# Performance work log

Hardware: AMD Instinct MI355X
Metric: run time of the kernel (lower is better)

## Reference

```python
import jax, jax.numpy as jnp
import numpy as np

D_K = 128
D_V = 128
SEQ_LEN = 2048


def setup_inputs() -> dict:
    key = jax.random.key(0)
    kq, kk, kv = jax.random.split(key, 3)
    q = jax.random.normal(kq, (SEQ_LEN, D_K), dtype=jnp.float32)
    k = jax.random.normal(kk, (SEQ_LEN, D_K), dtype=jnp.float32)
    v = jax.random.normal(kv, (SEQ_LEN, D_V), dtype=jnp.float32)
    return {"q": q, "k": k, "v": v}


def _step(carry, qkv):
    J, Svv, Sqv, Sqq, l = carry
    q, k, v = qkv
    l = l + 1
    fl = l.astype(J.dtype)
    # update_correlations: running means of outer products
    Svv = (fl - 1.0) / fl * Svv + jnp.outer(v, v) / fl
    Sqv = (fl - 1.0) / fl * Sqv + jnp.outer(q, v) / fl
    Sqq = (fl - 1.0) / fl * Sqq + jnp.outer(q, q) / fl

    first = l == 1

    # ecological params (J: [d_v, d_k], Sqv: [d_k, d_v], Sqq: [d_k, d_k])
    s_J = jnp.einsum('vk,kv->', J, Sqv)            # trace(J @ Sigma_qv)
    s_l = k @ Sqv @ v
    A_JJ = jnp.einsum('vk,kj,vj->', J, Sqq, J)     # trace(J Sqq J^T)
    A_ll = (v @ v) * (k @ Sqq @ k)
    A_Jl = v @ J @ Sqq @ k

    # safe denominators (unused branches must not produce NaN under where)
    A_JJ_s = jnp.where(first | (A_JJ == 0), 1.0, A_JJ)
    A_ll_s = jnp.where(first | (A_ll == 0), 1.0, A_ll)
    denom = A_JJ * A_ll - A_Jl ** 2
    denom_s = jnp.where(first | (denom == 0), 1.0, denom)

    margin = s_l - A_Jl * (s_J / A_JJ_s)

    wf = (A_ll * s_J - A_Jl * s_l) / denom_s
    wi = (A_JJ * s_l - A_Jl * s_J) / denom_s
    # nonnegativity constraints (check omega_i first, as in the source)
    wf_c = jnp.where(wi <= 0, s_J / A_JJ_s, jnp.where(wf <= 0, 0.0, wf))
    wi_c = jnp.where(wi <= 0, 0.0, jnp.where(wf <= 0, s_l / A_ll_s, wi))

    do_update = margin > 0
    vk = jnp.outer(v, k)
    J_upd = jnp.where(do_update, wf_c * J + wi_c * vk, J)
    J_new = jnp.where(first, vk, J_upd)
    updated = first | do_update

    # compute_cost with updated J and correlations
    cost = (0.5 * jnp.trace(Svv)
            - jnp.einsum('vk,kv->', J_new, Sqv)
            + 0.5 * jnp.einsum('vk,kj,vj->', J_new, Sqq, J_new))

    return (J_new, Svv, Sqv, Sqq, l), (cost, updated)


def _run(q, k, v):
    d_k, d_v = q.shape[-1], v.shape[-1]
    init = (jnp.zeros((d_v, d_k), q.dtype),
            jnp.zeros((d_v, d_v), q.dtype),
            jnp.zeros((d_k, d_v), q.dtype),
            jnp.zeros((d_k, d_k), q.dtype),
            jnp.int32(0))
    (J, _, _, _, _), (costs, updated) = jax.lax.scan(_step, init, (q, k, v))
    return costs, updated, J


def reference(q, k, v):
    return _run(q, k, v)
```

## Files before the change

kernel.cpp:

```cpp
#include <hip/hip_runtime.h>

#define SEQ 2048
#define D 128

typedef float v2f __attribute__((ext_vector_type(2)));
typedef float v4f __attribute__((ext_vector_type(4)));
#define LO2(v) __builtin_shufflevector(v, v, 0, 1)
#define HI2(v) __builtin_shufflevector(v, v, 2, 3)

__global__ __launch_bounds__(256) void precompute_kernel(
    const float* __restrict__ q, const float* __restrict__ k, const float* __restrict__ v,
    float* __restrict__ U, float* __restrict__ sl, float* __restrict__ kqq,
    float* __restrict__ vv, float* __restrict__ kq_adj, float* __restrict__ vv_adj,
    float* __restrict__ kU_adj, double* __restrict__ invl)
{
    const int s = blockIdx.x;
    const int tid = threadIdx.x;

    __shared__ float ks[D];
    __shared__ float vs[D];
    __shared__ float alpha[SEQ];
    __shared__ float red[8];
    __shared__ float upart[256];

    if (tid < D) ks[tid] = k[s * D + tid];
    else if (tid < 2 * D) vs[tid - D] = v[s * D + (tid - D)];
    __syncthreads();

    float p_a2 = 0.f, p_ab = 0.f;
    for (int i = tid; i <= s; i += 256) {
        const float4* qr = (const float4*)(q + (size_t)i * D);
        const float4* vr = (const float4*)(v + (size_t)i * D);
        float a = 0.f, b = 0.f;
#pragma unroll
        for (int j = 0; j < D / 4; ++j) {
            float4 q4 = qr[j];
            float4 v4 = vr[j];
            a += q4.x * ks[4 * j + 0] + q4.y * ks[4 * j + 1] + q4.z * ks[4 * j + 2] + q4.w * ks[4 * j + 3];
            b += v4.x * vs[4 * j + 0] + v4.y * vs[4 * j + 1] + v4.z * vs[4 * j + 2] + v4.w * vs[4 * j + 3];
        }
        alpha[i] = a;
        p_a2 += a * a;
        p_ab += a * b;
        if (i == s) vv[s] = b;
    }
#pragma unroll
    for (int off = 1; off < 64; off <<= 1) {
        p_a2 += __shfl_xor(p_a2, off);
        p_ab += __shfl_xor(p_ab, off);
    }
    const int wid = tid >> 6;
    if ((tid & 63) == 0) { red[wid] = p_a2; red[4 + wid] = p_ab; }
    __syncthreads();
    if (tid == 0) {
        kqq[s] = red[0] + red[1] + red[2] + red[3];
        sl[s]  = red[4] + red[5] + red[6] + red[7];
        invl[s] = 1.0 / (double)(s + 1);
    }

    if (tid < 64) {
        if (s + 1 < SEQ) {
            float p2 = ks[tid] * q[(size_t)(s + 1) * D + tid]
                     + ks[tid + 64] * q[(size_t)(s + 1) * D + 64 + tid];
#pragma unroll
            for (int off = 1; off < 64; off <<= 1) p2 += __shfl_xor(p2, off);
            if (tid == 0) kq_adj[s + 1] = p2;
        }
        if (s == 0 && tid == 0) { kq_adj[0] = 0.f; kU_adj[0] = 0.f; vv_adj[0] = 0.f; }
    } else if (tid < 128 && s > 0) {
        const int t2 = tid - 64;
        float p2 = vs[t2] * v[(size_t)(s - 1) * D + t2]
                 + vs[t2 + 64] * v[(size_t)(s - 1) * D + 64 + t2];
#pragma unroll
        for (int off = 1; off < 64; off <<= 1) p2 += __shfl_xor(p2, off);
        if (t2 == 0) vv_adj[s] = p2;
    }

    const int c = tid & (D - 1);
    const int h = tid >> 7;
    float a0 = 0.f, a1 = 0.f, a2 = 0.f, a3 = 0.f;
    int i = h;
    for (; i + 6 <= s; i += 8) {
        a0 = fmaf(q[(size_t)(i    ) * D + c], alpha[i    ], a0);
        a1 = fmaf(q[(size_t)(i + 2) * D + c], alpha[i + 2], a1);
        a2 = fmaf(q[(size_t)(i + 4) * D + c], alpha[i + 4], a2);
        a3 = fmaf(q[(size_t)(i + 6) * D + c], alpha[i + 6], a3);
    }
    for (; i <= s; i += 2) a0 = fmaf(q[(size_t)i * D + c], alpha[i], a0);
    upart[tid] = (a0 + a1) + (a2 + a3);
    __syncthreads();

    float kup = 0.f;
    if (tid < D) {
        const float uv = upart[tid] + upart[tid + D];
        U[(size_t)s * D + tid] = uv;
        if (s > 0) kup = uv * k[(size_t)(s - 1) * D + tid];
    }
#pragma unroll
    for (int off = 1; off < 64; off <<= 1) kup += __shfl_xor(kup, off);
    if (tid == 0)  red[0] = kup;
    if (tid == 64) red[1] = kup;
    __syncthreads();
    if (s > 0 && tid == 0) kU_adj[s] = red[0] + red[1];
}

#define DPP_ADD(x, ctrl) \
    ((x) + __int_as_float(__builtin_amdgcn_update_dpp(0, __float_as_int(x), (ctrl), 0xf, 0xf, true)))
#define REDUCE16(x) do { x = DPP_ADD(x, 0xB1); x = DPP_ADD(x, 0x4E); \
                         x = DPP_ADD(x, 0x141); x = DPP_ADD(x, 0x140); } while (0)

#define BARRIER() do { asm volatile("s_waitcnt lgkmcnt(0)" ::: "memory"); \
                       __builtin_amdgcn_s_barrier(); \
                       __builtin_amdgcn_sched_barrier(0); } while (0)

__global__ __launch_bounds__(1024, 4) void scan_kernel(
    const float* __restrict__ q, const float* __restrict__ k, const float* __restrict__ v,
    const float* __restrict__ U, const float* __restrict__ sl_arr,
    const float* __restrict__ kqq_arr, const float* __restrict__ vv_arr,
    const float* __restrict__ kq_adj, const float* __restrict__ vv_adj,
    const float* __restrict__ kU_adj, const double* __restrict__ invl_arr,
    float* __restrict__ out)
{
    const int tid  = threadIdx.x;
    const int lane = tid & 63;
    const int w    = __builtin_amdgcn_readfirstlane(tid >> 6);
    (void)kq_adj; (void)vv_adj; (void)kU_adj;

    __shared__ float ring[3][4][160];
    __shared__ __align__(16) float wred[3][32][4];
    __shared__ __align__(16) float fsl[SEQ];
    __shared__ __align__(16) float fkq[SEQ];
    __shared__ __align__(16) float fvv[SEQ];
    __shared__ __align__(16) double finv[SEQ];

    const bool isj     = (tid >= 512);
    const int  jw      = w - 8;
    const int  i16     = lane & 15;
    const int  r4      = lane >> 4;
    const int  o       = 20 * (i16 >> 1) + 8 * (i16 & 1);
    const int  rb      = (jw << 4) + (r4 << 2);
    const int  vo      = 20 * jw + (r4 << 2);

    const bool stager  = (tid >= 128) && (tid < 512);
    const int  which   = (tid >> 7) - 1;
    const int  sidx    = tid & 127;
    const int  widx    = ((sidx >> 4) * 20) + (sidx & 15);

    const bool vstager = (tid >= 64) && (tid < 128);
    const int  s2      = tid & 63;
    const int  vc0     = 2 * s2;
    const int  vwidx   = 20 * (vc0 >> 4) + (vc0 & 15);

    v2f jA0 = {0.f, 0.f}, jA1 = jA0, jA2 = jA0, jA3 = jA0;
    v2f jB0 = jA0, jB1 = jA0, jB2 = jA0, jB3 = jA0;
    v2f jC0 = jA0, jC1 = jA0, jC2 = jA0, jC3 = jA0;
    v2f jD0 = jA0, jD1 = jA0, jD2 = jA0, jD3 = jA0;

    float gs[3] = {0.f, 0.f, 0.f};
    v2f   gv[3] = {{0.f,0.f},{0.f,0.f},{0.f,0.f}};

    if (tid < 512) {
        ((float4*)fsl)[tid] = ((const float4*)sl_arr)[tid];
        ((float4*)fvv)[tid] = ((const float4*)vv_arr)[tid];
    } else {
        ((float4*)fkq)[tid - 512] = ((const float4*)kqq_arr)[tid - 512];
    }
    ((double2*)finv)[tid] = ((const double2*)invl_arr)[tid];

    if (stager) {
        if (which == 0) {
            ring[0][0][widx] = q[(size_t)1 * D + sidx];
            ring[1][0][widx] = q[(size_t)2 * D + sidx];
            gs[2] = q[(size_t)3 * D + sidx];
            gs[0] = q[(size_t)4 * D + sidx];
            gs[1] = q[(size_t)5 * D + sidx];
        } else if (which == 1) {
            ring[0][1][widx] = U[(size_t)1 * D + sidx];
            ring[1][1][widx] = U[(size_t)2 * D + sidx];
            gs[2] = U[(size_t)3 * D + sidx];
            gs[0] = U[(size_t)4 * D + sidx];
            gs[1] = U[(size_t)5 * D + sidx];
        } else {
            ring[0][2][widx] = k[(size_t)1 * D + sidx];
            ring[1][2][widx] = k[(size_t)2 * D + sidx];
            gs[2] = k[(size_t)3 * D + sidx];
            gs[0] = k[(size_t)4 * D + sidx];
            gs[1] = k[(size_t)5 * D + sidx];
        }
    } else if (vstager) {
        *(v2f*)&ring[0][3][vwidx] = *(const v2f*)&v[(size_t)1 * D + vc0];
        *(v2f*)&ring[1][3][vwidx] = *(const v2f*)&v[(size_t)2 * D + vc0];
        gv[2] = *(const v2f*)&v[(size_t)3 * D + vc0];
        gv[0] = *(const v2f*)&v[(size_t)4 * D + vc0];
        gv[1] = *(const v2f*)&v[(size_t)5 * D + vc0];
    }

    double SJ = 0.0, AJJ = 0.0, trSvv = 0.0;
    if (isj) {
        const v4f v0  = *(const v4f*)&v[rb];
        const v4f Ka0 = *(const v4f*)&k[8 * i16];
        const v4f Kb0 = *(const v4f*)&k[8 * i16 + 4];
        const v2f k0_ = LO2(Ka0), k1_ = HI2(Ka0), k2_ = LO2(Kb0), k3_ = HI2(Kb0);
        const v2f wA = {v0.x, v0.x}, wB = {v0.y, v0.y};
        const v2f wC = {v0.z, v0.z}, wD = {v0.w, v0.w};
        jA0 = wA * k0_; jA1 = wA * k1_; jA2 = wA * k2_; jA3 = wA * k3_;
        jB0 = wB * k0_; jB1 = wB * k1_; jB2 = wB * k2_; jB3 = wB * k3_;
        jC0 = wC * k0_; jC1 = wC * k1_; jC2 = wC * k2_; jC3 = wC * k3_;
        jD0 = wD * k0_; jD1 = wD * k1_; jD2 = wD * k2_; jD3 = wD * k3_;
        const double vv0 = (double)vv_arr[0];
        SJ    = (double)sl_arr[0];
        AJJ   = vv0 * (double)kqq_arr[0];
        trSvv = vv0;
    }
    if (tid == 0) {
        const double sl0 = (double)sl_arr[0];
        const double kq0 = (double)kqq_arr[0];
        const double vv0 = (double)vv_arr[0];
        out[0] = (float)((0.5 * vv0 - sl0 + 0.5 * vv0 * kq0) * invl_arr[0]);
        out[SEQ] = 1.f;
    }
    __syncthreads();

#define STEP_BODY(I, P, PN, PW)                                               \
{                                                                             \
    float c_sl = 0.f, c_kq = 0.f, c_vv = 0.f;                                 \
    double c_inv = 0.0;                                                       \
    v2f k0_ = {0.f, 0.f}, k1_ = k0_, k2_ = k0_, k3_ = k0_;                    \
    v4f vn4 = {0.f, 0.f, 0.f, 0.f};                                           \
    if (isj) {                                                                \
        c_sl = fsl[(I) + 1]; c_kq = fkq[(I) + 1]; c_vv = fvv[(I) + 1];        \
        c_inv = finv[(I) + 1];                                                \
        const v4f Qa = ((const v4f*)&ring[P][0][o])[0];                       \
        const v4f Qb = ((const v4f*)&ring[P][0][o])[1];                       \
        const v4f Ua = ((const v4f*)&ring[P][1][o])[0];                       \
        const v4f Ub = ((const v4f*)&ring[P][1][o])[1];                       \
        const v4f Ka = ((const v4f*)&ring[P][2][o])[0];                       \
        const v4f Kb = ((const v4f*)&ring[P][2][o])[1];                       \
        vn4 = *((const v4f*)&ring[P][3][vo]);                                 \
        k0_ = LO2(Ka); k1_ = HI2(Ka); k2_ = LO2(Kb); k3_ = HI2(Kb);           \
        const v2f q0 = LO2(Qa), q1 = HI2(Qa), q2 = LO2(Qb), q3 = HI2(Qb);     \
        v2f aA = jA0 * q0, aB = jB0 * q0, aC = jC0 * q0, aD = jD0 * q0;       \
        aA = __builtin_elementwise_fma(jA1, q1, aA);                          \
        aB = __builtin_elementwise_fma(jB1, q1, aB);                          \
        aC = __builtin_elementwise_fma(jC1, q1, aC);                          \
        aD = __builtin_elementwise_fma(jD1, q1, aD);                          \
        aA = __builtin_elementwise_fma(jA2, q2, aA);                          \
        aB = __builtin_elementwise_fma(jB2, q2, aB);                          \
        aC = __builtin_elementwise_fma(jC2, q2, aC);                          \
        aD = __builtin_elementwise_fma(jD2, q2, aD);                          \
        aA = __builtin_elementwise_fma(jA3, q3, aA);                          \
        aB = __builtin_elementwise_fma(jB3, q3, aB);                          \
        aC = __builtin_elementwise_fma(jC3, q3, aC);                          \
        aD = __builtin_elementwise_fma(jD3, q3, aD);                          \
        float YqA = aA.x + aA.y, YqB = aB.x + aB.y;                           \
        float YqC = aC.x + aC.y, YqD = aD.x + aD.y;                           \
        const v2f u0 = LO2(Ua), u1 = HI2(Ua), u2 = LO2(Ub), u3 = HI2(Ub);     \
        v2f bA = jA0 * u0, bB = jB0 * u0, bC = jC0 * u0, bD = jD0 * u0;       \
        bA = __builtin_elementwise_fma(jA1, u1, bA);                          \
        bB = __builtin_elementwise_fma(jB1, u1, bB);                          \
        bC = __builtin_elementwise_fma(jC1, u1, bC);                          \
        bD = __builtin_elementwise_fma(jD1, u1, bD);                          \
        bA = __builtin_elementwise_fma(jA2, u2, bA);                          \
        bB = __builtin_elementwise_fma(jB2, u2, bB);                          \
        bC = __builtin_elementwise_fma(jC2, u2, bC);                          \
        bD = __builtin_elementwise_fma(jD2, u2, bD);                          \
        bA = __builtin_elementwise_fma(jA3, u3, bA);                          \
        bB = __builtin_elementwise_fma(jB3, u3, bB);                          \
        bC = __builtin_elementwise_fma(jC3, u3, bC);                          \
        bD = __builtin_elementwise_fma(jD3, u3, bD);                          \
        float YwA = bA.x + bA.y, YwB = bB.x + bB.y;                           \
        float YwC = bC.x + bC.y, YwD = bD.x + bD.y;                           \
        REDUCE16(YqA); REDUCE16(YqB); REDUCE16(YqC); REDUCE16(YqD);           \
        REDUCE16(YwA); REDUCE16(YwB); REDUCE16(YwC); REDUCE16(YwD);           \
        const float z1 = (vn4.x * YqA + vn4.y * YqB) + (vn4.z * YqC + vn4.w * YqD); \
        const float z2 = (YqA * YqA + YqB * YqB) + (YqC * YqC + YqD * YqD);   \
        const float z4 = (vn4.x * YwA + vn4.y * YwB) + (vn4.z * YwC + vn4.w * YwD); \
        if ((lane & 15) == 15)                                                \
            *(float4*)&wred[P][(jw << 2) | r4][0] = make_float4(z1, z2, z4, 0.f); \
    }                                                                         \
    BARRIER();                                                                \
    if (stager) {                                                             \
        ring[PW][which][widx] = gs[PW];                                       \
        const int t6 = ((I) + 6 < SEQ) ? (I) + 6 : SEQ - 1;                   \
        gs[PW] = (which == 0) ? q[(size_t)t6 * D + sidx]                      \
               : (which == 1) ? U[(size_t)t6 * D + sidx]                      \
                              : k[(size_t)t6 * D + sidx];                     \
    } else if (vstager) {                                                     \
        *(v2f*)&ring[PW][3][vwidx] = gv[PW];                                  \
        const int t6 = ((I) + 6 < SEQ) ? (I) + 6 : SEQ - 1;                   \
        gv[PW] = *(const v2f*)&v[(size_t)t6 * D + vc0];                       \
    } else if (isj) {                                                         \
        const float4 wa = *(const float4*)&wred[P][lane & 15][0];             \
        const float4 wb = *(const float4*)&wred[P][16 + (lane & 15)][0];      \
        float wx = wa.x + wb.x, wy = wa.y + wb.y, wz = wa.z + wb.z;           \
        REDUCE16(wx);                                                         \
        REDUCE16(wy);                                                         \
        REDUCE16(wz);                                                         \
        trSvv += (double)c_vv;                                                \
        SJ    += (double)wx;                                                  \
        AJJ   += (double)wy;                                                  \
        const double AJl_ = (double)wz;                                       \
        const double s_l  = (double)c_sl;                                     \
        const double A_ll = (double)c_vv * (double)c_kq;                      \
        const double AJJ_s  = (AJJ == 0.0)  ? 1.0 : AJJ;                      \
        const double A_ll_s = (A_ll == 0.0) ? 1.0 : A_ll;                     \
        const double denom   = AJJ * A_ll - AJl_ * AJl_;                      \
        const double denom_s = (denom == 0.0) ? 1.0 : denom;                  \
        const double rden = 1.0 / denom_s;                                    \
        const double wf = (A_ll * SJ - AJl_ * s_l) * rden;                    \
        const double wi = (AJJ * s_l - AJl_ * SJ) * rden;                     \
        double wf_c, wi_c;                                                    \
        if (wi <= 0.0)      { wf_c = SJ / AJJ_s;  wi_c = 0.0; }               \
        else if (wf <= 0.0) { wf_c = 0.0;         wi_c = s_l / A_ll_s; }      \
        else                { wf_c = wf;          wi_c = wi; }                \
        const bool do_update = (s_l * AJJ_s - AJl_ * SJ) > 0.0;               \
        int mode = 0;                                                         \
        if (do_update) {                                                      \
            mode = 1;                                                         \
            const double nSJ = wf_c * SJ + wi_c * s_l;                        \
            AJJ = wf_c * wf_c * AJJ + 2.0 * wf_c * wi_c * AJl_                \
                + wi_c * wi_c * A_ll;                                         \
            SJ = nSJ;                                                         \
            const float uwf = (float)wf_c;                                    \
            const float uwi = (float)wi_c;                                    \
            const v2f wf2 = {uwf, uwf};                                       \
            const float sA = uwi * vn4.x, sB = uwi * vn4.y;                   \
            const float sC = uwi * vn4.z, sD = uwi * vn4.w;                   \
            const v2f wA = {sA, sA}, wB = {sB, sB};                           \
            const v2f wC = {sC, sC}, wD = {sD, sD};                           \
            jA0 = __builtin_elementwise_fma(jA0, wf2, wA * k0_);              \
            jA1 = __builtin_elementwise_fma(jA1, wf2, wA * k1_);              \
            jA2 = __builtin_elementwise_fma(jA2, wf2, wA * k2_);              \
            jA3 = __builtin_elementwise_fma(jA3, wf2, wA * k3_);              \
            jB0 = __builtin_elementwise_fma(jB0, wf2, wB * k0_);              \
            jB1 = __builtin_elementwise_fma(jB1, wf2, wB * k1_);              \
            jB2 = __builtin_elementwise_fma(jB2, wf2, wB * k2_);              \
            jB3 = __builtin_elementwise_fma(jB3, wf2, wB * k3_);              \
            jC0 = __builtin_elementwise_fma(jC0, wf2, wC * k0_);              \
            jC1 = __builtin_elementwise_fma(jC1, wf2, wC * k1_);              \
            jC2 = __builtin_elementwise_fma(jC2, wf2, wC * k2_);              \
            jC3 = __builtin_elementwise_fma(jC3, wf2, wC * k3_);              \
            jD0 = __builtin_elementwise_fma(jD0, wf2, wD * k0_);              \
            jD1 = __builtin_elementwise_fma(jD1, wf2, wD * k1_);              \
            jD2 = __builtin_elementwise_fma(jD2, wf2, wD * k2_);              \
            jD3 = __builtin_elementwise_fma(jD3, wf2, wD * k3_);              \
        }                                                                     \
        if (w == 8) {                                                         \
            const float cost = (float)((0.5 * trSvv - SJ + 0.5 * AJJ) * c_inv); \
            if (lane == 0) {                                                  \
                out[(I) + 1] = cost;                                          \
                out[SEQ + (I) + 1] = mode ? 1.f : 0.f;                        \
            }                                                                 \
        }                                                                     \
    }                                                                         \
}

    for (int i = 0; i + 2 < SEQ - 1; i += 3) {
        STEP_BODY(i,     0, 1, 2)
        STEP_BODY(i + 1, 1, 2, 0)
        STEP_BODY(i + 2, 2, 0, 1)
    }
    STEP_BODY(SEQ - 2, 0, 1, 2)
#undef STEP_BODY

    if (isj) {
        float* jb = out + 2 * SEQ + (size_t)rb * D + 8 * i16;
        *(v4f*)(jb + 0)         = __builtin_shufflevector(jA0, jA1, 0, 1, 2, 3);
        *(v4f*)(jb + 4)         = __builtin_shufflevector(jA2, jA3, 0, 1, 2, 3);
        *(v4f*)(jb + D + 0)     = __builtin_shufflevector(jB0, jB1, 0, 1, 2, 3);
        *(v4f*)(jb + D + 4)     = __builtin_shufflevector(jB2, jB3, 0, 1, 2, 3);
        *(v4f*)(jb + 2 * D + 0) = __builtin_shufflevector(jC0, jC1, 0, 1, 2, 3);
        *(v4f*)(jb + 2 * D + 4) = __builtin_shufflevector(jC2, jC3, 0, 1, 2, 3);
        *(v4f*)(jb + 3 * D + 0) = __builtin_shufflevector(jD0, jD1, 0, 1, 2, 3);
        *(v4f*)(jb + 3 * D + 4) = __builtin_shufflevector(jD2, jD3, 0, 1, 2, 3);
    }
}

extern "C" void kernel_launch(void* const* d_in, const int* in_sizes, int n_in,
                              void* d_out, int out_size, void* d_ws, size_t ws_size,
                              hipStream_t stream) {
    (void)in_sizes; (void)n_in; (void)out_size; (void)ws_size;
    const float* q = (const float*)d_in[0];
    const float* k = (const float*)d_in[1];
    const float* v = (const float*)d_in[2];
    float* out = (float*)d_out;

    float* U      = (float*)d_ws;
    float* sl     = U + (size_t)SEQ * D;
    float* kqq    = sl + SEQ;
    float* vv     = kqq + SEQ;
    float* kq_adj = vv + SEQ;
    float* vv_adj = kq_adj + SEQ;
    float* kU_adj = vv_adj + SEQ;
    double* invl  = (double*)(kU_adj + SEQ);

    precompute_kernel<<<SEQ, 256, 0, stream>>>(q, k, v, U, sl, kqq, vv,
                                               kq_adj, vv_adj, kU_adj, invl);
    scan_kernel<<<1, 1024, 0, stream>>>(q, k, v, U, sl, kqq, vv,
                                        kq_adj, vv_adj, kU_adj, invl, out);
}
```

Baseline: 2.606 ms.

## Process two scan steps per barrier round with deferred rank-2 J updates

Restructures the sequential scan so each round handles two timesteps. The precompute kernel now emits cross-step dot products (k·q, v·v, k·U at lags 1–3), which lets both steps' scalar decisions be derived from one batch of mat-vec reductions. The J update is deferred and applied as a fused rank-2 update. A Newton-refined hardware double reciprocal replaces the division. This halves the number of serial barrier rounds, at the cost of more LDS, more registers, extra precompute work and more complex algebra that could diverge numerically.

```diff
diff --git a/kernel.cpp b/kernel.cpp
--- a/kernel.cpp
+++ b/kernel.cpp
@@ -12,7 +12,8 @@
     const float* __restrict__ q, const float* __restrict__ k, const float* __restrict__ v,
     float* __restrict__ U, float* __restrict__ sl, float* __restrict__ kqq,
     float* __restrict__ vv, float* __restrict__ kq_adj, float* __restrict__ vv_adj,
-    float* __restrict__ kU_adj, double* __restrict__ invl)
+    float* __restrict__ kU_adj, double* __restrict__ invl,
+    float* __restrict__ kq_d, float* __restrict__ vv_d, float* __restrict__ kU_d)
 {
     const int s = blockIdx.x;
     const int tid = threadIdx.x;
@@ -59,21 +60,27 @@
     }
 
     if (tid < 64) {
-        if (s + 1 < SEQ) {
-            float p2 = ks[tid] * q[(size_t)(s + 1) * D + tid]
-                     + ks[tid + 64] * q[(size_t)(s + 1) * D + 64 + tid];
+        for (int d = 1; d <= 3; ++d) {
+            if (s + d < SEQ) {
+                float p2 = ks[tid] * q[(size_t)(s + d) * D + tid]
+                         + ks[tid + 64] * q[(size_t)(s + d) * D + 64 + tid];
 #pragma unroll
-            for (int off = 1; off < 64; off <<= 1) p2 += __shfl_xor(p2, off);
-            if (tid == 0) kq_adj[s + 1] = p2;
+                for (int off = 1; off < 64; off <<= 1) p2 += __shfl_xor(p2, off);
+                if (tid == 0) kq_d[(size_t)(s + d) * 3 + (d - 1)] = p2;
+            }
         }
         if (s == 0 && tid == 0) { kq_adj[0] = 0.f; kU_adj[0] = 0.f; vv_adj[0] = 0.f; }
-    } else if (tid < 128 && s > 0) {
+    } else if (tid < 128) {
         const int t2 = tid - 64;
-        float p2 = vs[t2] * v[(size_t)(s - 1) * D + t2]
-                 + vs[t2 + 64] * v[(size_t)(s - 1) * D + 64 + t2];
+        for (int d = 1; d <= 3; ++d) {
+            if (s - d >= 0) {
+                float p2 = vs[t2] * v[(size_t)(s - d) * D + t2]
+                         + vs[t2 + 64] * v[(size_t)(s - d) * D + 64 + t2];
 #pragma unroll
-        for (int off = 1; off < 64; off <<= 1) p2 += __shfl_xor(p2, off);
-        if (t2 == 0) vv_adj[s] = p2;
+                for (int off = 1; off < 64; off <<= 1) p2 += __shfl_xor(p2, off);
+                if (t2 == 0) vv_d[(size_t)s * 3 + (d - 1)] = p2;
+            }
+        }
     }
 
     const int c = tid & (D - 1);
@@ -90,18 +97,33 @@
     upart[tid] = (a0 + a1) + (a2 + a3);
     __syncthreads();
 
+    float uvv = 0.f;
     float kup = 0.f;
     if (tid < D) {
-        const float uv = upart[tid] + upart[tid + D];
-        U[(size_t)s * D + tid] = uv;
-        if (s > 0) kup = uv * k[(size_t)(s - 1) * D + tid];
+        uvv = upart[tid] + upart[tid + D];
+        U[(size_t)s * D + tid] = uvv;
+        if (s > 0) kup = uvv * k[(size_t)(s - 1) * D + tid];
     }
 #pragma unroll
     for (int off = 1; off < 64; off <<= 1) kup += __shfl_xor(kup, off);
     if (tid == 0)  red[0] = kup;
     if (tid == 64) red[1] = kup;
     __syncthreads();
-    if (s > 0 && tid == 0) kU_adj[s] = red[0] + red[1];
+    if (s > 0 && tid == 0) {
+        kU_adj[s] = red[0] + red[1];
+        kU_d[(size_t)s * 3 + 0] = red[0] + red[1];
+    }
+    for (int d = 2; d <= 3; ++d) {
+        float kd_ = 0.f;
+        if (tid < D && s - d >= 0) kd_ = uvv * k[(size_t)(s - d) * D + tid];
+#pragma unroll
+        for (int off = 1; off < 64; off <<= 1) kd_ += __shfl_xor(kd_, off);
+        __syncthreads();
+        if (tid == 0)  red[0] = kd_;
+        if (tid == 64) red[1] = kd_;
+        __syncthreads();
+        if (s - d >= 0 && tid == 0) kU_d[(size_t)s * 3 + (d - 1)] = red[0] + red[1];
+    }
 }
 
 #define DPP_ADD(x, ctrl) \
@@ -113,257 +135,364 @@
                        __builtin_amdgcn_s_barrier(); \
                        __builtin_amdgcn_sched_barrier(0); } while (0)
 
+static __device__ inline double fast_rcp(double d) {
+    double r;
+    asm("v_rcp_f64 %0, %1" : "=v"(r) : "v"(d));
+    double e = __builtin_fma(-d, r, 1.0); r = __builtin_fma(r, e, r);
+    e = __builtin_fma(-d, r, 1.0); r = __builtin_fma(r, e, r);
+    return r;
+}
+
 __global__ __launch_bounds__(1024, 4) void scan_kernel(
     const float* __restrict__ q, const float* __restrict__ k, const float* __restrict__ v,
     const float* __restrict__ U, const float* __restrict__ sl_arr,
     const float* __restrict__ kqq_arr, const float* __restrict__ vv_arr,
-    const float* __restrict__ kq_adj, const float* __restrict__ vv_adj,
-    const float* __restrict__ kU_adj, const double* __restrict__ invl_arr,
+    const float* __restrict__ qd_arr, const float* __restrict__ vvd_arr,
+    const float* __restrict__ kud_arr, const double* __restrict__ invl_arr,
     float* __restrict__ out)
 {
     const int tid  = threadIdx.x;
     const int lane = tid & 63;
     const int w    = __builtin_amdgcn_readfirstlane(tid >> 6);
-    (void)kq_adj; (void)vv_adj; (void)kU_adj;
-
-    __shared__ float ring[3][4][160];
-    __shared__ __align__(16) float wred[3][32][4];
-    __shared__ __align__(16) float fsl[SEQ];
-    __shared__ __align__(16) float fkq[SEQ];
-    __shared__ __align__(16) float fvv[SEQ];
+
+    __shared__ float ring[3][8][160];
+    __shared__ __align__(16) float wred[3][32][12];
+    __shared__ __align__(16) float decLDS[3][4];
+    __shared__ float fsl[SEQ];
+    __shared__ float fkq[SEQ];
+    __shared__ float fvv[SEQ];
+    __shared__ float fqd[SEQ * 3];
+    __shared__ float fvd[SEQ * 3];
+    __shared__ float fkd[SEQ * 3];
     __shared__ __align__(16) double finv[SEQ];
 
-    const bool isj     = (tid >= 512);
-    const int  jw      = w - 8;
-    const int  i16     = lane & 15;
-    const int  r4      = lane >> 4;
-    const int  o       = 20 * (i16 >> 1) + 8 * (i16 & 1);
-    const int  rb      = (jw << 4) + (r4 << 2);
-    const int  vo      = 20 * jw + (r4 << 2);
-
-    const bool stager  = (tid >= 128) && (tid < 512);
-    const int  which   = (tid >> 7) - 1;
-    const int  sidx    = tid & 127;
-    const int  widx    = ((sidx >> 4) * 20) + (sidx & 15);
-
-    const bool vstager = (tid >= 64) && (tid < 128);
-    const int  s2      = tid & 63;
-    const int  vc0     = 2 * s2;
-    const int  vwidx   = 20 * (vc0 >> 4) + (vc0 & 15);
+    const bool isj = (tid >= 512);
+    const int  jw  = w - 8;
+    const int  i16 = lane & 15;
+    const int  r4  = lane >> 4;
+    const int  o   = 20 * (i16 >> 1) + 8 * (i16 & 1);
+    const int  rb  = (jw << 4) + (r4 << 2);
+    const int  vo  = 20 * jw + (r4 << 2);
+
+    const bool stager = (tid >= 64 && tid < 256) || (tid >= 320 && tid < 512);
+    const int  st     = (tid < 256) ? tid - 64 : tid - 128;
+
+    if (tid < 512) {
+        ((float4*)fsl)[tid] = ((const float4*)sl_arr)[tid];
+        ((float4*)fkq)[tid] = ((const float4*)kqq_arr)[tid];
+        ((float4*)fvv)[tid] = ((const float4*)vv_arr)[tid];
+    }
+    ((double2*)finv)[tid] = ((const double2*)invl_arr)[tid];
+    for (int i = tid; i < SEQ * 3 / 4; i += 1024) {
+        ((float4*)fqd)[i] = ((const float4*)qd_arr)[i];
+        ((float4*)fvd)[i] = ((const float4*)vvd_arr)[i];
+        ((float4*)fkd)[i] = ((const float4*)kud_arr)[i];
+    }
 
     v2f jA0 = {0.f, 0.f}, jA1 = jA0, jA2 = jA0, jA3 = jA0;
     v2f jB0 = jA0, jB1 = jA0, jB2 = jA0, jB3 = jA0;
     v2f jC0 = jA0, jC1 = jA0, jC2 = jA0, jC3 = jA0;
     v2f jD0 = jA0, jD1 = jA0, jD2 = jA0, jD3 = jA0;
-
-    float gs[3] = {0.f, 0.f, 0.f};
-    v2f   gv[3] = {{0.f,0.f},{0.f,0.f},{0.f,0.f}};
-
-    if (tid < 512) {
-        ((float4*)fsl)[tid] = ((const float4*)sl_arr)[tid];
-        ((float4*)fvv)[tid] = ((const float4*)vv_arr)[tid];
-    } else {
-        ((float4*)fkq)[tid - 512] = ((const float4*)kqq_arr)[tid - 512];
-    }
-    ((double2*)finv)[tid] = ((const double2*)invl_arr)[tid];
+    v4f Q1a = {0,0,0,0}, Q1b = Q1a, Q2a = Q1a, Q2b = Q1a;
+    v4f U1a = Q1a, U1b = Q1a, U2a = Q1a, U2b = Q1a;
+    v4f kA1a = Q1a, kA1b = Q1a, kA2a = Q1a, kA2b = Q1a;
+    v4f kB1a = Q1a, kB1b = Q1a, kB2a = Q1a, kB2b = Q1a;
+    v4f vA1 = Q1a, vA2 = Q1a, vB1 = Q1a, vB2 = Q1a;
+
+    float g0[3] = {0, 0, 0}, g1[3] = {0, 0, 0}, g2[3] = {0, 0, 0};
+
+    double SJ = 0.0, AJJ = 0.0, trSvv = 0.0;
+    double fa = 1.0, ga = 0.0, fb = 1.0, gb = 0.0;
+
+#define MATVEC(Xa, Xb, RA, RB, RC, RD)                                        \
+    {                                                                         \
+        const v2f x0 = LO2(Xa), x1 = HI2(Xa), x2 = LO2(Xb), x3 = HI2(Xb);     \
+        v2f tA = jA0 * x0, tB = jB0 * x0, tC = jC0 * x0, tD = jD0 * x0;       \
+        tA = __builtin_elementwise_fma(jA1, x1, tA);                          \
+        tB = __builtin_elementwise_fma(jB1, x1, tB);                          \
+        tC = __builtin_elementwise_fma(jC1, x1, tC);                          \
+        tD = __builtin_elementwise_fma(jD1, x1, tD);                          \
+        tA = __builtin_elementwise_fma(jA2, x2, tA);                          \
+        tB = __builtin_elementwise_fma(jB2, x2, tB);                          \
+        tC = __builtin_elementwise_fma(jC2, x2, tC);                          \
+        tD = __builtin_elementwise_fma(jD2, x2, tD);                          \
+        tA = __builtin_elementwise_fma(jA3, x3, tA);                          \
+        tB = __builtin_elementwise_fma(jB3, x3, tB);                          \
+        tC = __builtin_elementwise_fma(jC3, x3, tC);                          \
+        tD = __builtin_elementwise_fma(jD3, x3, tD);                          \
+        RA = tA.x + tA.y; RB = tB.x + tB.y; RC = tC.x + tC.y; RD = tD.x + tD.y; \
+    }
+
+#define DOTPHASE(P_)                                                          \
+    {                                                                         \
+        float Yq1A, Yq1B, Yq1C, Yq1D, Yq2A, Yq2B, Yq2C, Yq2D;                 \
+        float W1A, W1B, W1C, W1D, W2A, W2B, W2C, W2D;                         \
+        MATVEC(Q1a, Q1b, Yq1A, Yq1B, Yq1C, Yq1D)                              \
+        MATVEC(Q2a, Q2b, Yq2A, Yq2B, Yq2C, Yq2D)                              \
+        MATVEC(U1a, U1b, W1A, W1B, W1C, W1D)                                  \
+        MATVEC(U2a, U2b, W2A, W2B, W2C, W2D)                                  \
+        REDUCE16(Yq1A); REDUCE16(Yq1B); REDUCE16(Yq1C); REDUCE16(Yq1D);       \
+        REDUCE16(Yq2A); REDUCE16(Yq2B); REDUCE16(Yq2C); REDUCE16(Yq2D);       \
+        float pb11 = vB1.x * Yq1A + vB1.y * Yq1B + vB1.z * Yq1C + vB1.w * Yq1D; \
+        float pb21 = Yq1A * Yq1A + Yq1B * Yq1B + Yq1C * Yq1C + Yq1D * Yq1D;   \
+        float pb41 = vB1.x * W1A + vB1.y * W1B + vB1.z * W1C + vB1.w * W1D;   \
+        REDUCE16(pb41);                                                       \
+        float pg11 = vA1.x * Yq1A + vA1.y * Yq1B + vA1.z * Yq1C + vA1.w * Yq1D; \
+        float pg21 = vA2.x * Yq1A + vA2.y * Yq1B + vA2.z * Yq1C + vA2.w * Yq1D; \
+        float pb12 = vB2.x * Yq2A + vB2.y * Yq2B + vB2.z * Yq2C + vB2.w * Yq2D; \
+        float pb22 = Yq2A * Yq2A + Yq2B * Yq2B + Yq2C * Yq2C + Yq2D * Yq2D;   \
+        float pb42 = vB2.x * W2A + vB2.y * W2B + vB2.z * W2C + vB2.w * W2D;   \
+        REDUCE16(pb42);                                                       \
+        float pg12 = vA1.x * Yq2A + vA1.y * Yq2B + vA1.z * Yq2C + vA1.w * Yq2D; \
+        float pg22 = vA2.x * Yq2A + vA2.y * Yq2B + vA2.z * Yq2C + vA2.w * Yq2D; \
+        float pg3  = vB1.x * Yq2A + vB1.y * Yq2B + vB1.z * Yq2C + vB1.w * Yq2D; \
+        if ((lane & 15) == 15) {                                              \
+            const int e_ = (jw << 2) | r4;                                    \
+            *(float4*)&wred[P_][e_][0] = make_float4(pb11, pb21, pb41, pg11); \
+            *(float4*)&wred[P_][e_][4] = make_float4(pg21, pb12, pb22, pb42); \
+            *(float4*)&wred[P_][e_][8] = make_float4(pg12, pg22, pg3, 0.f);   \
+        }                                                                     \
+    }
+
+#define J_UPDATE(PW_)                                                         \
+    {                                                                         \
+        const float4 df_ = *(const float4*)&decLDS[PW_][0];                   \
+        const float F_ = df_.x, Ga_ = df_.y, Gb_ = df_.z;                     \
+        if (!(F_ == 1.f && Ga_ == 0.f && Gb_ == 0.f)) {                       \
+            const v2f F2_ = {F_, F_};                                         \
+            const v2f k10 = LO2(kA1a), k11 = HI2(kA1a), k12 = LO2(kA1b), k13 = HI2(kA1b); \
+            const v2f k20 = LO2(kA2a), k21 = HI2(kA2a), k22 = LO2(kA2b), k23 = HI2(kA2b); \
+            { const float w1 = Ga_ * vA1.x, w2 = Gb_ * vA2.x;                 \
+              const v2f w1_ = {w1, w1}, w2_ = {w2, w2};                       \
+              jA0 = __builtin_elementwise_fma(jA0, F2_, __builtin_elementwise_fma(w1_, k10, w2_ * k20)); \
+              jA1 = __builtin_elementwise_fma(jA1, F2_, __builtin_elementwise_fma(w1_, k11, w2_ * k21)); \
+              jA2 = __builtin_elementwise_fma(jA2, F2_, __builtin_elementwise_fma(w1_, k12, w2_ * k22)); \
+              jA3 = __builtin_elementwise_fma(jA3, F2_, __builtin_elementwise_fma(w1_, k13, w2_ * k23)); } \
+            { const float w1 = Ga_ * vA1.y, w2 = Gb_ * vA2.y;                 \
+              const v2f w1_ = {w1, w1}, w2_ = {w2, w2};                       \
+              jB0 = __builtin_elementwise_fma(jB0, F2_, __builtin_elementwise_fma(w1_, k10, w2_ * k20)); \
+              jB1 = __builtin_elementwise_fma(jB1, F2_, __builtin_elementwise_fma(w1_, k11, w2_ * k21)); \
+              jB2 = __builtin_elementwise_fma(jB2, F2_, __builtin_elementwise_fma(w1_, k12, w2_ * k22)); \
+              jB3 = __builtin_elementwise_fma(jB3, F2_, __builtin_elementwise_fma(w1_, k13, w2_ * k23)); } \
+            { const float w1 = Ga_ * vA1.z, w2 = Gb_ * vA2.z;                 \
+              const v2f w1_ = {w1, w1}, w2_ = {w2, w2};                       \
+              jC0 = __builtin_elementwise_fma(jC0, F2_, __builtin_elementwise_fma(w1_, k10, w2_ * k20)); \
+              jC1 = __builtin_elementwise_fma(jC1, F2_, __builtin_elementwise_fma(w1_, k11, w2_ * k21)); \
+              jC2 = __builtin_elementwise_fma(jC2, F2_, __builtin_elementwise_fma(w1_, k12, w2_ * k22)); \
+              jC3 = __builtin_elementwise_fma(jC3, F2_, __builtin_elementwise_fma(w1_, k13, w2_ * k23)); } \
+            { const float w1 = Ga_ * vA1.w, w2 = Gb_ * vA2.w;                 \
+              const v2f w1_ = {w1, w1}, w2_ = {w2, w2};                       \
+              jD0 = __builtin_elementwise_fma(jD0, F2_, __builtin_elementwise_fma(w1_, k10, w2_ * k20)); \
+              jD1 = __builtin_elementwise_fma(jD1, F2_, __builtin_elementwise_fma(w1_, k11, w2_ * k21)); \
+              jD2 = __builtin_elementwise_fma(jD2, F2_, __builtin_elementwise_fma(w1_, k12, w2_ * k22)); \
+              jD3 = __builtin_elementwise_fma(jD3, F2_, __builtin_elementwise_fma(w1_, k13, w2_ * k23)); } \
+        }                                                                     \
+    }
+
+#define DECIDE(S_L, A_LL, AJL, FO, GO, MO)                                    \
+    {                                                                         \
+        const double s_l_ = (S_L), A_ll_ = (A_LL), AJl_ = (AJL);              \
+        const double AJJ_s_ = (AJJ == 0.0) ? 1.0 : AJJ;                       \
+        const double A_ll_s_ = (A_ll_ == 0.0) ? 1.0 : A_ll_;                  \
+        const double denom_ = AJJ * A_ll_ - AJl_ * AJl_;                      \
+        const double denom_s_ = (denom_ == 0.0) ? 1.0 : denom_;               \
+        const double rden_ = fast_rcp(denom_s_);                              \
+        const double wf_ = (A_ll_ * SJ - AJl_ * s_l_) * rden_;                \
+        const double wi_ = (AJJ * s_l_ - AJl_ * SJ) * rden_;                  \
+        double wfc_, wic_;                                                    \
+        if (wi_ <= 0.0)      { wfc_ = SJ / AJJ_s_;  wic_ = 0.0; }             \
+        else if (wf_ <= 0.0) { wfc_ = 0.0;          wic_ = s_l_ / A_ll_s_; }  \
+        else                 { wfc_ = wf_;          wic_ = wi_; }             \
+        if ((s_l_ * AJJ_s_ - AJl_ * SJ) > 0.0) {                              \
+            MO = 1;                                                           \
+            const double nSJ_ = wfc_ * SJ + wic_ * s_l_;                      \
+            AJJ = wfc_ * wfc_ * AJJ + 2.0 * wfc_ * wic_ * AJl_                \
+                + wic_ * wic_ * A_ll_;                                        \
+            SJ = nSJ_; FO = wfc_; GO = wic_;                                  \
+        } else { MO = 0; FO = 1.0; GO = 0.0; }                                \
+    }
+
+#define DECIDER(R, P_, PW_, LAST)                                             \
+    {                                                                         \
+        const int s1 = 2 * (R) + 1;                                           \
+        const int s2c = ((LAST)) ? SEQ - 1 : 2 * (R) + 2;                     \
+        const int la = lane & 15;                                             \
+        const float4 e0 = *(const float4*)&wred[PW_][la][0];                  \
+        const float4 e1 = *(const float4*)&wred[PW_][la][4];                  \
+        const float4 e2 = *(const float4*)&wred[PW_][la][8];                  \
+        const float4 h0 = *(const float4*)&wred[PW_][16 + la][0];             \
+        const float4 h1 = *(const float4*)&wred[PW_][16 + la][4];             \
+        const float4 h2 = *(const float4*)&wred[PW_][16 + la][8];             \
+        float B1_1 = e0.x + h0.x, B2_1 = e0.y + h0.y, B4_1 = e0.z + h0.z;     \
+        float G1_1 = e0.w + h0.w, G2_1 = e1.x + h1.x, B1_2 = e1.y + h1.y;     \
+        float B2_2 = e1.z + h1.z, B4_2 = e1.w + h1.w, G1_2 = e2.x + h2.x;     \
+        float G2_2 = e2.y + h2.y, G3f = e2.z + h2.z;                          \
+        REDUCE16(B1_1); REDUCE16(B2_1); REDUCE16(B4_1); REDUCE16(G1_1);       \
+        REDUCE16(G2_1); REDUCE16(B1_2); REDUCE16(B2_2); REDUCE16(B4_2);       \
+        REDUCE16(G1_2); REDUCE16(G2_2); REDUCE16(G3f);                        \
+        const int ia = (s1 >= 2) ? s1 - 2 : 0;                                \
+        const double vva = (double)fvv[ia];                                   \
+        const double vvb = (double)fvv[s1 - 1];                               \
+        const double vab = (double)fvd[(s1 - 1) * 3 + 0];                     \
+        const double qd1_1 = (double)fqd[s1 * 3 + 0], qd1_2 = (double)fqd[s1 * 3 + 1]; \
+        const double vd1_1 = (double)fvd[s1 * 3 + 0], vd1_2 = (double)fvd[s1 * 3 + 1]; \
+        const double kd1_1 = (double)fkd[s1 * 3 + 0], kd1_2 = (double)fkd[s1 * 3 + 1]; \
+        const double sl1 = (double)fsl[s1], kq1 = (double)fkq[s1], vv1 = (double)fvv[s1]; \
+        const double qd2_1 = (double)fqd[s2c * 3 + 0], qd2_2 = (double)fqd[s2c * 3 + 1], qd2_3 = (double)fqd[s2c * 3 + 2]; \
+        const double vd2_1 = (double)fvd[s2c * 3 + 0], vd2_2 = (double)fvd[s2c * 3 + 1], vd2_3 = (double)fvd[s2c * 3 + 2]; \
+        const double kd2_1 = (double)fkd[s2c * 3 + 0], kd2_2 = (double)fkd[s2c * 3 + 1], kd2_3 = (double)fkd[s2c * 3 + 2]; \
+        const double sl2 = (double)fsl[s2c], kq2 = (double)fkq[s2c], vv2 = (double)fvv[s2c]; \
+        const double inv1 = finv[s1], inv2 = finv[s2c];                       \
+        const double A = fa * fb, Ca = fb * ga, Cb = gb;                      \
+        const double z1 = A * (double)B1_1 + Ca * (vd1_2 * qd1_2)             \
+                        + Cb * (vd1_1 * qd1_1);                               \
+        const double z2 = A * A * (double)B2_1                                \
+                        + Ca * Ca * qd1_2 * qd1_2 * vva                       \
+                        + Cb * Cb * qd1_1 * qd1_1 * vvb                       \
+                        + 2.0 * A * (Ca * qd1_2 * (double)G1_1                \
+                                     + Cb * qd1_1 * (double)G2_1)             \
+                        + 2.0 * Ca * Cb * qd1_2 * qd1_1 * vab;                \
+        const double z4 = A * (double)B4_1 + Ca * vd1_2 * kd1_2               \
+                        + Cb * vd1_1 * kd1_1;                                 \
+        SJ += z1; AJJ += z2; trSvv += vv1;                                    \
+        double f1, g1; int mode1;                                             \
+        DECIDE(sl1, vv1 * kq1, z4, f1, g1, mode1)                             \
+        const double cost1 = (0.5 * trSvv - SJ + 0.5 * AJJ) * inv1;           \
+        const double A2 = f1 * A, Ca2 = f1 * Ca, Cb2 = f1 * Cb, Cc2 = g1;     \
+        double f2 = 1.0, g2 = 0.0; int mode2 = 0; double cost2 = 0.0;         \
+        if (!(LAST)) {                                                        \
+            const double y1 = A2 * (double)B1_2 + Ca2 * vd2_3 * qd2_3         \
+                            + Cb2 * vd2_2 * qd2_2 + Cc2 * vd2_1 * qd2_1;      \
+            const double y2 = A2 * A2 * (double)B2_2                          \
+                            + Ca2 * Ca2 * qd2_3 * qd2_3 * vva                 \
+                            + Cb2 * Cb2 * qd2_2 * qd2_2 * vvb                 \
+                            + Cc2 * Cc2 * qd2_1 * qd2_1 * vv1                 \
+                            + 2.0 * A2 * (Ca2 * qd2_3 * (double)G1_2          \
+                                          + Cb2 * qd2_2 * (double)G2_2        \
+                                          + Cc2 * qd2_1 * (double)G3f)        \
+                            + 2.0 * (Ca2 * Cb2 * qd2_3 * qd2_2 * vab          \
+                                     + Ca2 * Cc2 * qd2_3 * qd2_1 * vd1_2      \
+                                     + Cb2 * Cc2 * qd2_2 * qd2_1 * vd1_1);    \
+            const double y4 = A2 * (double)B4_2 + Ca2 * vd2_3 * kd2_3         \
+                            + Cb2 * vd2_2 * kd2_2 + Cc2 * vd2_1 * kd2_1;      \
+            SJ += y1; AJJ += y2; trSvv += vv2;                                \
+            DECIDE(sl2, vv2 * kq2, y4, f2, g2, mode2)                         \
+            cost2 = (0.5 * trSvv - SJ + 0.5 * AJJ) * inv2;                    \
+        }                                                                     \
+        fa = f1; ga = g1; fb = f2; gb = g2;                                   \
+        if (lane == 0) {                                                      \
+            out[s1] = (float)cost1; out[SEQ + s1] = mode1 ? 1.f : 0.f;        \
+            if (!(LAST)) {                                                    \
+                out[s2c] = (float)cost2; out[SEQ + s2c] = mode2 ? 1.f : 0.f;  \
+            }                                                                 \
+            *(float4*)&decLDS[P_][0] = make_float4(                           \
+                (float)(f1 * f2), (float)(g1 * f2), (float)g2, 0.f);          \
+        }                                                                     \
+    }
+
+#define ST_ONE(SLOT, GARR, R, PW_)                                            \
+    { const int s_ = (SLOT); const int a_ = s_ >> 7, c_ = s_ & 127;           \
+      const int wix = (c_ >> 4) * 20 + (c_ & 15);                             \
+      ring[PW_][a_][wix] = GARR[PW_];                                         \
+      const float* b_ = (a_ < 2) ? q : (a_ < 4) ? U : (a_ < 6) ? k : v;       \
+      int stp = 2 * ((R) + 6) + 1 + (a_ & 1);                                 \
+      if (stp > SEQ - 1) stp = SEQ - 1;                                       \
+      GARR[PW_] = b_[(size_t)stp * D + c_]; }
+
+#define STAGE(R, PW_)                                                         \
+    {                                                                         \
+        ST_ONE(st, g0, R, PW_)                                                \
+        ST_ONE(st + 384, g1, R, PW_)                                          \
+        if (st < 256) ST_ONE(st + 768, g2, R, PW_)                            \
+    }
+
+#define ROUND(R, P_, PN_, PW_, LAST)                                          \
+    {                                                                         \
+        if (isj) {                                                            \
+            J_UPDATE(PW_)                                                     \
+            vA1 = vB1; vA2 = vB2;                                             \
+            kA1a = kB1a; kA1b = kB1b; kA2a = kB2a; kA2b = kB2b;               \
+            Q1a = ((const v4f*)&ring[P_][0][o])[0];                           \
+            Q1b = ((const v4f*)&ring[P_][0][o])[1];                           \
+            Q2a = ((const v4f*)&ring[P_][1][o])[0];                           \
+            Q2b = ((const v4f*)&ring[P_][1][o])[1];                           \
+            U1a = ((const v4f*)&ring[P_][2][o])[0];                           \
+            U1b = ((const v4f*)&ring[P_][2][o])[1];                           \
+            U2a = ((const v4f*)&ring[P_][3][o])[0];                           \
+            U2b = ((const v4f*)&ring[P_][3][o])[1];                           \
+            kB1a = ((const v4f*)&ring[P_][4][o])[0];                          \
+            kB1b = ((const v4f*)&ring[P_][4][o])[1];                          \
+            kB2a = ((const v4f*)&ring[P_][5][o])[0];                          \
+            kB2b = ((const v4f*)&ring[P_][5][o])[1];                          \
+            vB1 = *(const v4f*)&ring[P_][6][vo];                              \
+            vB2 = *(const v4f*)&ring[P_][7][vo];                              \
+            DOTPHASE(P_)                                                      \
+        } else if (w == 0) {                                                  \
+            DECIDER(R, P_, PW_, LAST)                                         \
+        } else if (stager) {                                                  \
+            STAGE(R, PW_)                                                     \
+        }                                                                     \
+        BARRIER();                                                            \
+    }
+
+#define PRO_ONE(SLOT, GARR)                                                   \
+    { const int s_ = (SLOT); const int a_ = s_ >> 7, c_ = s_ & 127;           \
+      const int wix = (c_ >> 4) * 20 + (c_ & 15);                             \
+      const float* b_ = (a_ < 2) ? q : (a_ < 4) ? U : (a_ < 6) ? k : v;       \
+      const int o_ = (a_ & 1);                                                \
+      ring[0][a_][wix] = b_[(size_t)(3 + o_) * D + c_];                       \
+      ring[1][a_][wix] = b_[(size_t)(5 + o_) * D + c_];                       \
+      GARR[2] = b_[(size_t)(7 + o_) * D + c_];                                \
+      GARR[0] = b_[(size_t)(9 + o_) * D + c_];                                \
+      GARR[1] = b_[(size_t)(11 + o_) * D + c_]; }
 
     if (stager) {
-        if (which == 0) {
-            ring[0][0][widx] = q[(size_t)1 * D + sidx];
-            ring[1][0][widx] = q[(size_t)2 * D + sidx];
-            gs[2] = q[(size_t)3 * D + sidx];
-            gs[0] = q[(size_t)4 * D + sidx];
-            gs[1] = q[(size_t)5 * D + sidx];
-        } else if (which == 1) {
-            ring[0][1][widx] = U[(size_t)1 * D + sidx];
-            ring[1][1][widx] = U[(size_t)2 * D + sidx];
-            gs[2] = U[(size_t)3 * D + sidx];
-            gs[0] = U[(size_t)4 * D + sidx];
-            gs[1] = U[(size_t)5 * D + sidx];
-        } else {
-            ring[0][2][widx] = k[(size_t)1 * D + sidx];
-            ring[1][2][widx] = k[(size_t)2 * D + sidx];
-            gs[2] = k[(size_t)3 * D + sidx];
-            gs[0] = k[(size_t)4 * D + sidx];
-            gs[1] = k[(size_t)5 * D + sidx];
-        }
-    } else if (vstager) {
-        *(v2f*)&ring[0][3][vwidx] = *(const v2f*)&v[(size_t)1 * D + vc0];
-        *(v2f*)&ring[1][3][vwidx] = *(const v2f*)&v[(size_t)2 * D + vc0];
-        gv[2] = *(const v2f*)&v[(size_t)3 * D + vc0];
-        gv[0] = *(const v2f*)&v[(size_t)4 * D + vc0];
-        gv[1] = *(const v2f*)&v[(size_t)5 * D + vc0];
-    }
-
-    double SJ = 0.0, AJJ = 0.0, trSvv = 0.0;
-    if (isj) {
+        PRO_ONE(st, g0)
+        PRO_ONE(st + 384, g1)
+        if (st < 256) PRO_ONE(st + 768, g2)
+    } else if (isj) {
         const v4f v0  = *(const v4f*)&v[rb];
-        const v4f Ka0 = *(const v4f*)&k[8 * i16];
-        const v4f Kb0 = *(const v4f*)&k[8 * i16 + 4];
-        const v2f k0_ = LO2(Ka0), k1_ = HI2(Ka0), k2_ = LO2(Kb0), k3_ = HI2(Kb0);
+        const v4f K0a = *(const v4f*)&k[8 * i16];
+        const v4f K0b = *(const v4f*)&k[8 * i16 + 4];
+        const v2f k0_ = LO2(K0a), k1_ = HI2(K0a), k2_ = LO2(K0b), k3_ = HI2(K0b);
         const v2f wA = {v0.x, v0.x}, wB = {v0.y, v0.y};
         const v2f wC = {v0.z, v0.z}, wD = {v0.w, v0.w};
         jA0 = wA * k0_; jA1 = wA * k1_; jA2 = wA * k2_; jA3 = wA * k3_;
         jB0 = wB * k0_; jB1 = wB * k1_; jB2 = wB * k2_; jB3 = wB * k3_;
         jC0 = wC * k0_; jC1 = wC * k1_; jC2 = wC * k2_; jC3 = wC * k3_;
         jD0 = wD * k0_; jD1 = wD * k1_; jD2 = wD * k2_; jD3 = wD * k3_;
+        Q1a = *(const v4f*)&q[D + 8 * i16];     Q1b = *(const v4f*)&q[D + 8 * i16 + 4];
+        Q2a = *(const v4f*)&q[2 * D + 8 * i16]; Q2b = *(const v4f*)&q[2 * D + 8 * i16 + 4];
+        U1a = *(const v4f*)&U[D + 8 * i16];     U1b = *(const v4f*)&U[D + 8 * i16 + 4];
+        U2a = *(const v4f*)&U[2 * D + 8 * i16]; U2b = *(const v4f*)&U[2 * D + 8 * i16 + 4];
+        kB1a = *(const v4f*)&k[D + 8 * i16];     kB1b = *(const v4f*)&k[D + 8 * i16 + 4];
+        kB2a = *(const v4f*)&k[2 * D + 8 * i16]; kB2b = *(const v4f*)&k[2 * D + 8 * i16 + 4];
+        vB1 = *(const v4f*)&v[D + rb];
+        vB2 = *(const v4f*)&v[2 * D + rb];
+        DOTPHASE(2)
+    } else if (w == 0) {
+        SJ = (double)sl_arr[0];
         const double vv0 = (double)vv_arr[0];
-        SJ    = (double)sl_arr[0];
-        AJJ   = vv0 * (double)kqq_arr[0];
+        AJJ = vv0 * (double)kqq_arr[0];
         trSvv = vv0;
-    }
-    if (tid == 0) {
-        const double sl0 = (double)sl_arr[0];
-        const double kq0 = (double)kqq_arr[0];
-        const double vv0 = (double)vv_arr[0];
-        out[0] = (float)((0.5 * vv0 - sl0 + 0.5 * vv0 * kq0) * invl_arr[0]);
-        out[SEQ] = 1.f;
+        fa = 1.0; ga = 0.0; fb = 1.0; gb = 0.0;
+        if (lane == 0) {
+            out[0] = (float)((0.5 * trSvv - SJ + 0.5 * AJJ) * invl_arr[0]);
+            out[SEQ] = 1.f;
+            decLDS[2][0] = 1.f; decLDS[2][1] = 0.f; decLDS[2][2] = 0.f; decLDS[2][3] = 0.f;
+        }
     }
     __syncthreads();
 
-#define STEP_BODY(I, P, PN, PW)                                               \
-{                                                                             \
-    float c_sl = 0.f, c_kq = 0.f, c_vv = 0.f;                                 \
-    double c_inv = 0.0;                                                       \
-    v2f k0_ = {0.f, 0.f}, k1_ = k0_, k2_ = k0_, k3_ = k0_;                    \
-    v4f vn4 = {0.f, 0.f, 0.f, 0.f};                                           \
-    if (isj) {                                                                \
-        c_sl = fsl[(I) + 1]; c_kq = fkq[(I) + 1]; c_vv = fvv[(I) + 1];        \
-        c_inv = finv[(I) + 1];                                                \
-        const v4f Qa = ((const v4f*)&ring[P][0][o])[0];                       \
-        const v4f Qb = ((const v4f*)&ring[P][0][o])[1];                       \
-        const v4f Ua = ((const v4f*)&ring[P][1][o])[0];                       \
-        const v4f Ub = ((const v4f*)&ring[P][1][o])[1];                       \
-        const v4f Ka = ((const v4f*)&ring[P][2][o])[0];                       \
-        const v4f Kb = ((const v4f*)&ring[P][2][o])[1];                       \
-        vn4 = *((const v4f*)&ring[P][3][vo]);                                 \
-        k0_ = LO2(Ka); k1_ = HI2(Ka); k2_ = LO2(Kb); k3_ = HI2(Kb);           \
-        const v2f q0 = LO2(Qa), q1 = HI2(Qa), q2 = LO2(Qb), q3 = HI2(Qb);     \
-        v2f aA = jA0 * q0, aB = jB0 * q0, aC = jC0 * q0, aD = jD0 * q0;       \
-        aA = __builtin_elementwise_fma(jA1, q1, aA);                          \
-        aB = __builtin_elementwise_fma(jB1, q1, aB);                          \
-        aC = __builtin_elementwise_fma(jC1, q1, aC);                          \
-        aD = __builtin_elementwise_fma(jD1, q1, aD);                          \
-        aA = __builtin_elementwise_fma(jA2, q2, aA);                          \
-        aB = __builtin_elementwise_fma(jB2, q2, aB);                          \
-        aC = __builtin_elementwise_fma(jC2, q2, aC);                          \
-        aD = __builtin_elementwise_fma(jD2, q2, aD);                          \
-        aA = __builtin_elementwise_fma(jA3, q3, aA);                          \
-        aB = __builtin_elementwise_fma(jB3, q3, aB);                          \
-        aC = __builtin_elementwise_fma(jC3, q3, aC);                          \
-        aD = __builtin_elementwise_fma(jD3, q3, aD);                          \
-        float YqA = aA.x + aA.y, YqB = aB.x + aB.y;                           \
-        float YqC = aC.x + aC.y, YqD = aD.x + aD.y;                           \
-        const v2f u0 = LO2(Ua), u1 = HI2(Ua), u2 = LO2(Ub), u3 = HI2(Ub);     \
-        v2f bA = jA0 * u0, bB = jB0 * u0, bC = jC0 * u0, bD = jD0 * u0;       \
-        bA = __builtin_elementwise_fma(jA1, u1, bA);                          \
-        bB = __builtin_elementwise_fma(jB1, u1, bB);                          \
-        bC = __builtin_elementwise_fma(jC1, u1, bC);                          \
-        bD = __builtin_elementwise_fma(jD1, u1, bD);                          \
-        bA = __builtin_elementwise_fma(jA2, u2, bA);                          \
-        bB = __builtin_elementwise_fma(jB2, u2, bB);                          \
-        bC = __builtin_elementwise_fma(jC2, u2, bC);                          \
-        bD = __builtin_elementwise_fma(jD2, u2, bD);                          \
-        bA = __builtin_elementwise_fma(jA3, u3, bA);                          \
-        bB = __builtin_elementwise_fma(jB3, u3, bB);                          \
-        bC = __builtin_elementwise_fma(jC3, u3, bC);                          \
-        bD = __builtin_elementwise_fma(jD3, u3, bD);                          \
-        float YwA = bA.x + bA.y, YwB = bB.x + bB.y;                           \
-        float YwC = bC.x + bC.y, YwD = bD.x + bD.y;                           \
-        REDUCE16(YqA); REDUCE16(YqB); REDUCE16(YqC); REDUCE16(YqD);           \
-        REDUCE16(YwA); REDUCE16(YwB); REDUCE16(YwC); REDUCE16(YwD);           \
-        const float z1 = (vn4.x * YqA + vn4.y * YqB) + (vn4.z * YqC + vn4.w * YqD); \
-        const float z2 = (YqA * YqA + YqB * YqB) + (YqC * YqC + YqD * YqD);   \
-        const float z4 = (vn4.x * YwA + vn4.y * YwB) + (vn4.z * YwC + vn4.w * YwD); \
-        if ((lane & 15) == 15)                                                \
-            *(float4*)&wred[P][(jw << 2) | r4][0] = make_float4(z1, z2, z4, 0.f); \
-    }                                                                         \
-    BARRIER();                                                                \
-    if (stager) {                                                             \
-        ring[PW][which][widx] = gs[PW];                                       \
-        const int t6 = ((I) + 6 < SEQ) ? (I) + 6 : SEQ - 1;                   \
-        gs[PW] = (which == 0) ? q[(size_t)t6 * D + sidx]                      \
-               : (which == 1) ? U[(size_t)t6 * D + sidx]                      \
-                              : k[(size_t)t6 * D + sidx];                     \
-    } else if (vstager) {                                                     \
-        *(v2f*)&ring[PW][3][vwidx] = gv[PW];                                  \
-        const int t6 = ((I) + 6 < SEQ) ? (I) + 6 : SEQ - 1;                   \
-        gv[PW] = *(const v2f*)&v[(size_t)t6 * D + vc0];                       \
-    } else if (isj) {                                                         \
-        const float4 wa = *(const float4*)&wred[P][lane & 15][0];             \
-        const float4 wb = *(const float4*)&wred[P][16 + (lane & 15)][0];      \
-        float wx = wa.x + wb.x, wy = wa.y + wb.y, wz = wa.z + wb.z;           \
-        REDUCE16(wx);                                                         \
-        REDUCE16(wy);                                                         \
-        REDUCE16(wz);                                                         \
-        trSvv += (double)c_vv;                                                \
-        SJ    += (double)wx;                                                  \
-        AJJ   += (double)wy;                                                  \
-        const double AJl_ = (double)wz;                                       \
-        const double s_l  = (double)c_sl;                                     \
-        const double A_ll = (double)c_vv * (double)c_kq;                      \
-        const double AJJ_s  = (AJJ == 0.0)  ? 1.0 : AJJ;                      \
-        const double A_ll_s = (A_ll == 0.0) ? 1.0 : A_ll;                     \
-        const double denom   = AJJ * A_ll - AJl_ * AJl_;                      \
-        const double denom_s = (denom == 0.0) ? 1.0 : denom;                  \
-        const double rden = 1.0 / denom_s;                                    \
-        const double wf = (A_ll * SJ - AJl_ * s_l) * rden;                    \
-        const double wi = (AJJ * s_l - AJl_ * SJ) * rden;                     \
-        double wf_c, wi_c;                                                    \
-        if (wi <= 0.0)      { wf_c = SJ / AJJ_s;  wi_c = 0.0; }               \
-        else if (wf <= 0.0) { wf_c = 0.0;         wi_c = s_l / A_ll_s; }      \
-        else                { wf_c = wf;          wi_c = wi; }                \
-        const bool do_update = (s_l * AJJ_s - AJl_ * SJ) > 0.0;               \
-        int mode = 0;                                                         \
-        if (do_update) {                                                      \
-            mode = 1;                                                         \
-            const double nSJ = wf_c * SJ + wi_c * s_l;                        \
-            AJJ = wf_c * wf_c * AJJ + 2.0 * wf_c * wi_c * AJl_                \
-                + wi_c * wi_c * A_ll;                                         \
-            SJ = nSJ;                                                         \
-            const float uwf = (float)wf_c;                                    \
-            const float uwi = (float)wi_c;                                    \
-            const v2f wf2 = {uwf, uwf};                                       \
-            const float sA = uwi * vn4.x, sB = uwi * vn4.y;                   \
-            const float sC = uwi * vn4.z, sD = uwi * vn4.w;                   \
-            const v2f wA = {sA, sA}, wB = {sB, sB};                           \
-            const v2f wC = {sC, sC}, wD = {sD, sD};                           \
-            jA0 = __builtin_elementwise_fma(jA0, wf2, wA * k0_);              \
-            jA1 = __builtin_elementwise_fma(jA1, wf2, wA * k1_);              \
-            jA2 = __builtin_elementwise_fma(jA2, wf2, wA * k2_);              \
-            jA3 = __builtin_elementwise_fma(jA3, wf2, wA * k3_);              \
-            jB0 = __builtin_elementwise_fma(jB0, wf2, wB * k0_);              \
-            jB1 = __builtin_elementwise_fma(jB1, wf2, wB * k1_);              \
-            jB2 = __builtin_elementwise_fma(jB2, wf2, wB * k2_);              \
-            jB3 = __builtin_elementwise_fma(jB3, wf2, wB * k3_);              \
-            jC0 = __builtin_elementwise_fma(jC0, wf2, wC * k0_);              \
-            jC1 = __builtin_elementwise_fma(jC1, wf2, wC * k1_);              \
-            jC2 = __builtin_elementwise_fma(jC2, wf2, wC * k2_);              \
-            jC3 = __builtin_elementwise_fma(jC3, wf2, wC * k3_);              \
-            jD0 = __builtin_elementwise_fma(jD0, wf2, wD * k0_);              \
-            jD1 = __builtin_elementwise_fma(jD1, wf2, wD * k1_);              \
-            jD2 = __builtin_elementwise_fma(jD2, wf2, wD * k2_);              \
-            jD3 = __builtin_elementwise_fma(jD3, wf2, wD * k3_);              \
-        }                                                                     \
-        if (w == 8) {                                                         \
-            const float cost = (float)((0.5 * trSvv - SJ + 0.5 * AJJ) * c_inv); \
-            if (lane == 0) {                                                  \
-                out[(I) + 1] = cost;                                          \
-                out[SEQ + (I) + 1] = mode ? 1.f : 0.f;                        \
-            }                                                                 \
-        }                                                                     \
-    }                                                                         \
-}
-
-    for (int i = 0; i + 2 < SEQ - 1; i += 3) {
-        STEP_BODY(i,     0, 1, 2)
-        STEP_BODY(i + 1, 1, 2, 0)
-        STEP_BODY(i + 2, 2, 0, 1)
-    }
-    STEP_BODY(SEQ - 2, 0, 1, 2)
-#undef STEP_BODY
+    for (int r = 0; r < 1023; r += 3) {
+        ROUND(r,     0, 1, 2, false)
+        ROUND(r + 1, 1, 2, 0, false)
+        ROUND(r + 2, 2, 0, 1, false)
+    }
+    ROUND(1023, 0, 1, 2, true)
 
     if (isj) {
+        J_UPDATE(0)
         float* jb = out + 2 * SEQ + (size_t)rb * D + 8 * i16;
         *(v4f*)(jb + 0)         = __builtin_shufflevector(jA0, jA1, 0, 1, 2, 3);
         *(v4f*)(jb + 4)         = __builtin_shufflevector(jA2, jA3, 0, 1, 2, 3);
@@ -393,9 +522,14 @@
     float* vv_adj = kq_adj + SEQ;
     float* kU_adj = vv_adj + SEQ;
     double* invl  = (double*)(kU_adj + SEQ);
-
+    float* kq_d   = (float*)(invl + SEQ);
+    float* vv_d   = kq_d + (size_t)SEQ * 3;
+    float* kU_d   = vv_d + (size_t)SEQ * 3;
+
+    hipMemsetAsync(kq_d, 0, 3 * (size_t)SEQ * 3 * sizeof(float), stream);
     precompute_kernel<<<SEQ, 256, 0, stream>>>(q, k, v, U, sl, kqq, vv,
-                                               kq_adj, vv_adj, kU_adj, invl);
+                                               kq_adj, vv_adj, kU_adj, invl,
+                                               kq_d, vv_d, kU_d);
     scan_kernel<<<1, 1024, 0, stream>>>(q, k, v, U, sl, kqq, vv,
-                                        kq_adj, vv_adj, kU_adj, invl, out);
+                                        kq_d, vv_d, kU_d, invl, out);
 }
```

After: 5.170 ms. +98.4%, slower.
